# Kernel optimization log

Measured on AMD Instinct MI355X. Metric: run time of the kernel, lower is better.

## Reference

```python
import jax, jax.numpy as jnp
import numpy as np
from jax.scipy.linalg import solve_triangular

S = 64            # number of weight samples (Xi.shape[0])
OUT = 256         # out_channels
IN_CH, K = 64, 3
F = IN_CH * K * K # in_features == inducing_batch == 576
LOG_PREC_INIT = -4.0
LOG_PREC_LR = 1.0


def setup_inputs() -> dict:
    key = jax.random.key(0)
    k1, k2, k3, k4 = jax.random.split(key, 4)
    Xi = jax.random.normal(k1, (S, 128, F), jnp.float32)          # only shape[0] is used
    Xi_param = jax.random.normal(k2, (1, F, F), jnp.float32)      # self.Xi: [1, inducing_batch, in_features]
    u = jax.random.normal(k3, (OUT, F, 1), jnp.float32)           # self.u
    log_prec_scaled = (LOG_PREC_INIT / LOG_PREC_LR) * jnp.ones((1, 1, F), jnp.float32)
    Z = jax.random.normal(k4, (S, OUT, F, 1), jnp.float32)        # internal randn noise, made explicit
    return dict(Xi=Xi, Xi_param=Xi_param, u=u, log_prec_scaled=log_prec_scaled, Z=Z)


def reference(Xi, Xi_param, u, log_prec_scaled, Z):
    S_ = Xi.shape[0]
    Fd = Xi_param.shape[-1]
    O = u.shape[0]
    # log_prec = log_prec_lr * log_prec_scaled  (precs == 1)
    log_prec = LOG_PREC_LR * log_prec_scaled[0]                    # [1, F]
    Xe = jnp.broadcast_to(Xi_param, (S_, Fd, Fd))                  # [S, I, F]
    XiLT = jnp.exp(log_prec) * jnp.swapaxes(Xe, -1, -2)            # [S, F, I]  (prec_L is None branch)
    XiLXi = XiLT @ Xe                                              # [S, F, F]
    XiLY = jnp.einsum('sfi,oi->sfo', XiLT, u[..., 0])              # [S, F, O]  (torch: [S, O, F, 1])
    # NealPrior over in_shape: precision = fan_in * I, fan_in = in_features
    prior_prec = float(Fd)
    prec = XiLXi + prior_prec * jnp.eye(Fd, dtype=XiLXi.dtype)     # [S, F, F]
    L = jnp.linalg.cholesky(prec)
    logdet_prec = 2.0 * jnp.sum(jnp.log(jnp.diagonal(L, axis1=-2, axis2=-1)), -1)  # [S]
    logdet_prec_tot = O * logdet_prec                              # expand(S, O).sum(-1)
    # cholesky_solve(XiLY, L): prec^{-1} XiLY, batched over O via RHS columns
    mean = solve_triangular(L, solve_triangular(L, XiLY, lower=True), lower=True, trans=1)  # [S, F, O]
    Zm = jnp.swapaxes(Z[..., 0], -1, -2)                           # [S, F, O]
    dW = solve_triangular(L, Zm, lower=True, trans=1)              # L^T dW = Z
    sample_fo = mean + dW                                          # [S, F, O]
    sample = jnp.swapaxes(sample_fo, -1, -2)                       # [S, O, F] == self._sample
    # logP = mvnormal_log_prob_unnorm(prior_prec, sample^T):  -0.5 tr(x^T P x) + 0.5*O*logdet(P)
    logP = (-0.5 * prior_prec * jnp.sum(sample_fo ** 2, (-1, -2))
            + 0.5 * O * Fd * jnp.log(jnp.asarray(prior_prec, sample.dtype)))
    logQ = -0.5 * jnp.sum(Z ** 2, (-1, -2, -3)) + 0.5 * logdet_prec_tot
    logpq = logP - logQ                                            # [S]
    return sample, logpq
```

## Files before the change

kernel.cpp:

```cpp
#include <hip/hip_runtime.h>

#define F 576
#define OUTC 256
#define SNUM 64
#define PP 576.0f
#define NBLK 36

typedef unsigned short u16;
typedef __attribute__((ext_vector_type(8))) short short8;
typedef __attribute__((ext_vector_type(4))) float f32x4;

__device__ __forceinline__ u16 f2b_rne(float x) {
  unsigned u = __float_as_uint(x);
  unsigned r = (u + 0x7FFF + ((u >> 16) & 1)) >> 16;
  return (u16)r;
}

__device__ __forceinline__ void gbar(int* cnt, int* gen, int b, int barid) {
  __syncthreads();
  if (threadIdx.x == 0) {
    __builtin_amdgcn_fence(__ATOMIC_RELEASE, "agent");
    __hip_atomic_fetch_add(cnt, 1, __ATOMIC_RELAXED, __HIP_MEMORY_SCOPE_AGENT);
    if (b == 0) {
      int target = barid * NBLK;
      while (__hip_atomic_load(cnt, __ATOMIC_RELAXED, __HIP_MEMORY_SCOPE_AGENT) < target) {
        __builtin_amdgcn_s_sleep(1);
      }
      __builtin_amdgcn_fence(__ATOMIC_ACQUIRE, "agent");
      __builtin_amdgcn_fence(__ATOMIC_RELEASE, "agent");
      __hip_atomic_store(gen, barid, __ATOMIC_RELAXED, __HIP_MEMORY_SCOPE_AGENT);
    } else {
      while (__hip_atomic_load(gen, __ATOMIC_RELAXED, __HIP_MEMORY_SCOPE_AGENT) < barid) {
        __builtin_amdgcn_s_sleep(1);
      }
    }
    __builtin_amdgcn_fence(__ATOMIC_ACQUIRE, "agent");
  }
  __syncthreads();
}

__device__ __forceinline__ void mm16(const float (*As)[68], const float (*Bs)[68],
                                     float acc[4][4], int tx, int ty) {
#pragma unroll
  for (int k = 0; k < 32; ++k) {
    float4 a4 = *(const float4*)&As[k][ty * 4];
    float4 b4 = *(const float4*)&Bs[k][tx * 4];
    float av[4] = {a4.x, a4.y, a4.z, a4.w};
    float bv[4] = {b4.x, b4.y, b4.z, b4.w};
#pragma unroll
    for (int r = 0; r < 4; ++r)
#pragma unroll
      for (int c = 0; c < 4; ++c) acc[r][c] += av[r] * bv[c];
  }
}

__device__ void tile_gemm(const float* __restrict__ A, int lda,
                          const float* __restrict__ B, int ldb,
                          float* __restrict__ C, int ldc,
                          int m0, int n0, int K, float sgn,
                          float (*As)[68], float (*Bs)[68]) {
  int t = threadIdx.x, tx = t & 15, ty = t >> 4;
  float acc[4][4] = {};
  for (int k0 = 0; k0 < K; k0 += 32) {
    int rr = t >> 2, kq = t & 3;
    const float* ap = &A[(m0 + rr) * lda + k0 + kq * 8];
    float4 a0 = *(const float4*)ap;
    float4 a1 = *(const float4*)(ap + 4);
    As[kq*8+0][rr] = a0.x; As[kq*8+1][rr] = a0.y;
    As[kq*8+2][rr] = a0.z; As[kq*8+3][rr] = a0.w;
    As[kq*8+4][rr] = a1.x; As[kq*8+5][rr] = a1.y;
    As[kq*8+6][rr] = a1.z; As[kq*8+7][rr] = a1.w;
    int col = t & 63, kr = t >> 6;
#pragma unroll
    for (int kk = 0; kk < 32; kk += 4)
      Bs[kr + kk][col] = B[(k0 + kr + kk) * ldb + n0 + col];
    __syncthreads();
    mm16(As, Bs, acc, tx, ty);
    __syncthreads();
  }
#pragma unroll
  for (int r = 0; r < 4; ++r)
#pragma unroll
    for (int c = 0; c < 4; ++c)
      C[(m0 + ty*4 + r) * ldc + n0 + tx*4 + c] = sgn * acc[r][c];
}

__device__ void diag_factor(float* Ts ) {
  int t = threadIdx.x;
  __syncthreads();
  if (t < 64) {
    int l = t;
    float r[64];
#pragma unroll
    for (int g = 0; g < 64; ++g) r[g] = Ts[l*66 + g];
#pragma unroll
    for (int j = 0; j < 64; ++j) {
      float d = __shfl(r[j], j, 64);
      float inv = 1.0f / sqrtf(d);
      float c = r[j] * inv;
      r[j] = c;
#pragma unroll
      for (int g = j + 1; g < 64; ++g)
        r[g] = fmaf(-__shfl(c, g, 64), c, r[g]);
    }
#pragma unroll
    for (int g = 0; g < 64; ++g) Ts[l*66 + g] = r[g];
  }
  __syncthreads();
}

__device__ void panel_phase(float* __restrict__ G, int k0, int b,
                            float* Ts, float* invd) {
  int t = threadIdx.x;
  for (int idx = t; idx < 64 * 64; idx += 256) {
    int i = idx >> 6, j = idx & 63;
    Ts[i*66 + j] = G[(k0 + i) * F + k0 + j];
  }
  __syncthreads();
  if (t < 64) invd[t] = 1.0f / Ts[t*66 + t];
  __syncthreads();
  int l = t & 63, w = t >> 6;
  int r0 = k0 + 64 + b * 16 + w * 4;
  float v0 = G[(r0 + 0) * F + k0 + l];
  float v1 = G[(r0 + 1) * F + k0 + l];
  float v2 = G[(r0 + 2) * F + k0 + l];
  float v3 = G[(r0 + 3) * F + k0 + l];
#pragma unroll
  for (int j = 0; j < 64; ++j) {
    float dj = invd[j];
    float x0 = __shfl(v0, j, 64) * dj;
    float x1 = __shfl(v1, j, 64) * dj;
    float x2 = __shfl(v2, j, 64) * dj;
    float x3 = __shfl(v3, j, 64) * dj;
    if (l > j) {
      float lj = Ts[l*66 + j];
      v0 = fmaf(-x0, lj, v0);
      v1 = fmaf(-x1, lj, v1);
      v2 = fmaf(-x2, lj, v2);
      v3 = fmaf(-x3, lj, v3);
    }
  }
  float dl = invd[l];
  G[(r0 + 0) * F + k0 + l] = v0 * dl;
  G[(r0 + 1) * F + k0 + l] = v1 * dl;
  G[(r0 + 2) * F + k0 + l] = v2 * dl;
  G[(r0 + 3) * F + k0 + l] = v3 * dl;
}

__device__ void upd_phase(float* __restrict__ G, int k0, int ti, int tj, bool fuse,
                          float (*As)[68], float (*Bs)[68], float* Ts) {
  int b0 = k0 + 64;
  int i0 = b0 + ti * 64, j0 = b0 + tj * 64;
  int t = threadIdx.x, tx = t & 15, ty = t >> 4;
  float acc[4][4] = {};
  for (int kk0 = 0; kk0 < 64; kk0 += 32) {
    for (int idx = t; idx < 64 * 32; idx += 256) {
      int ii = idx >> 5, kk = idx & 31;
      As[kk][ii] = G[(i0 + ii) * F + k0 + kk0 + kk];
      Bs[kk][ii] = G[(j0 + ii) * F + k0 + kk0 + kk];
    }
    __syncthreads();
#pragma unroll
    for (int k = 0; k < 32; ++k) {
      float a[4], b[4];
#pragma unroll
      for (int m = 0; m < 4; ++m) { a[m] = As[k][ty*4 + m]; b[m] = Bs[k][tx*4 + m]; }
#pragma unroll
      for (int r = 0; r < 4; ++r)
#pragma unroll
        for (int c = 0; c < 4; ++c) acc[r][c] += a[r] * b[c];
    }
    __syncthreads();
  }
  if (!fuse) {
#pragma unroll
    for (int r = 0; r < 4; ++r)
#pragma unroll
      for (int c = 0; c < 4; ++c)
        G[(i0 + ty*4 + r) * F + j0 + tx*4 + c] -= acc[r][c];
  } else {
#pragma unroll
    for (int r = 0; r < 4; ++r)
#pragma unroll
      for (int c = 0; c < 4; ++c)
        Ts[(ty*4 + r)*66 + tx*4 + c] =
            G[(i0 + ty*4 + r) * F + j0 + tx*4 + c] - acc[r][c];
    diag_factor(Ts);
    for (int idx = t; idx < 64 * 64; idx += 256) {
      int i = idx >> 6, j = idx & 63;
      if (j <= i) G[(i0 + i) * F + j0 + j] = Ts[i*66 + j];
    }
  }
}

__device__ void base_inv_phase(const float* __restrict__ G, float* __restrict__ LI,
                               int blk, float* Ts, float* invd) {
  int base = blk * 64, t = threadIdx.x;
  for (int idx = t; idx < 64 * 64; idx += 256) {
    int i = idx >> 6, j = idx & 63;
    Ts[i*66 + j] = G[(base + i) * F + base + j];
  }
  __syncthreads();
  if (t < 64) invd[t] = 1.0f / Ts[t*66 + t];
  __syncthreads();
  int l = t & 63, w = t >> 6;
  float v[16];
#pragma unroll
  for (int c = 0; c < 16; ++c) v[c] = (l == (w * 16 + c)) ? 1.0f : 0.0f;
#pragma unroll
  for (int j = 0; j < 64; ++j) {
    float dj = invd[j];
    float lj = (l > j) ? Ts[l*66 + j] : 0.0f;
#pragma unroll
    for (int c = 0; c < 16; ++c) {
      float x = __shfl(v[c], j, 64) * dj;
      v[c] = fmaf(-x, lj, v[c]);
    }
  }
  float dl = invd[l];
#pragma unroll
  for (int c = 0; c < 16; ++c)
    LI[(base + l) * F + base + w * 16 + c] = v[c] * dl;
}

__device__ void mean_phase(const float* __restrict__ LI, const float* __restrict__ T,
                           float* __restrict__ meanT, int bf, int bo,
                           float (*As)[68], float (*Bs)[68]) {
  int t = threadIdx.x, tx = t & 15, ty = t >> 4;
  int f0 = bf * 64, o0 = bo * 64;
  float acc[4][4] = {};
  for (int g0 = f0; g0 < F; g0 += 32) {
    int col = t & 63, kr = t >> 6;
#pragma unroll
    for (int kk = 0; kk < 32; kk += 4) {
      As[kr + kk][col] = T[(g0 + kr + kk) * OUTC + o0 + col];
      Bs[kr + kk][col] = LI[(g0 + kr + kk) * F + f0 + col];
    }
    __syncthreads();
    mm16(As, Bs, acc, tx, ty);
    __syncthreads();
  }
#pragma unroll
  for (int r = 0; r < 4; ++r) {
    float4 st = make_float4(acc[r][0], acc[r][1], acc[r][2], acc[r][3]);
    *(float4*)&meanT[(o0 + ty*4 + r) * F + f0 + tx*4] = st;
  }
}

__global__ __launch_bounds__(256) void k_mid(float* __restrict__ G, float* __restrict__ LI,
                                             const float* __restrict__ Yb,
                                             float* __restrict__ Tb, float* __restrict__ meanT,
                                             int* __restrict__ cnt, int* __restrict__ gen) {
  __shared__ float As[32][68];
  __shared__ float Bs[32][68];
  __shared__ float Ts[64 * 66];
  __shared__ float invd[64];
  int bar = 0;
  int b = blockIdx.x, t = threadIdx.x;
  float* Tw = Tb;

  if (b == 0) {
    for (int idx = t; idx < 64 * 64; idx += 256) {
      int i = idx >> 6, j = idx & 63;
      Ts[i*66 + j] = G[i * F + j];
    }
    diag_factor(Ts);
    for (int idx = t; idx < 64 * 64; idx += 256) {
      int i = idx >> 6, j = idx & 63;
      if (j <= i) G[i * F + j] = Ts[i*66 + j];
    }
  }
  gbar(cnt, gen, b, ++bar);

  for (int k = 0; k < 8; ++k) {
    int k0 = k * 64;
    int n = 512 - k0;
    if (b < n / 16) panel_phase(G, k0, b, Ts, invd);
    gbar(cnt, gen, b, ++bar);
    int nt = n / 64, ntiles = nt * (nt + 1) / 2;
    if (b < ntiles) {
      int ti = 0, bb = b;
      while (bb >= ti + 1) { bb -= ti + 1; ++ti; }
      int tj = bb;
      upd_phase(G, k0, ti, tj, (ti == 0 && tj == 0), As, Bs, Ts);
    }
    gbar(cnt, gen, b, ++bar);
  }

  if (b < 9) {
    base_inv_phase(G, LI, b, Ts, invd);
  } else {
    int m = b - 9;
    for (int q = m; q < 72; q += 27) {
      int r = q / 8, cc = q % 8;
      int c = cc + (cc >= r ? 1 : 0);
      for (int idx = t; idx < 64 * 16; idx += 256) {
        int i = idx >> 4, jj = idx & 15;
        ((float4*)&LI[(r * 64 + i) * F + c * 64])[jj] = make_float4(0.f, 0.f, 0.f, 0.f);
      }
    }
  }
  gbar(cnt, gen, b, ++bar);

  if (b < 4) {
    tile_gemm(G + 64*F + b*128*(F+1), F, LI + b*128*(F+1), F,
              Tw + b*4096, 64, 0, 0, 64, 1.0f, As, Bs);
    tile_gemm(LI + 64*(F+1) + b*128*(F+1), F, Tw + b*4096, 64,
              LI + 64*F + b*128*(F+1), F, 0, 0, 64, -1.0f, As, Bs);
  }
  gbar(cnt, gen, b, ++bar);
  if (b < 8) {
    int z = b >> 2, tl = b & 3;
    tile_gemm(G + 128*F + z*256*(F+1), F, LI + z*256*(F+1), F,
              Tw + z*16384, 128, (tl>>1)*64, (tl&1)*64, 128, 1.0f, As, Bs);
  }
  gbar(cnt, gen, b, ++bar);
  if (b < 8) {
    int z = b >> 2, tl = b & 3;
    tile_gemm(LI + 128*(F+1) + z*256*(F+1), F, Tw + z*16384, 128,
              LI + 128*F + z*256*(F+1), F, (tl>>1)*64, (tl&1)*64, 128, -1.0f, As, Bs);
  }
  gbar(cnt, gen, b, ++bar);
  if (b < 16) tile_gemm(G + 256*F, F, LI, F, Tw, 256,
                        (b>>2)*64, (b&3)*64, 256, 1.0f, As, Bs);
  gbar(cnt, gen, b, ++bar);
  if (b < 16) tile_gemm(LI + 256*(F+1), F, Tw, 256, LI + 256*F, F,
                        (b>>2)*64, (b&3)*64, 256, -1.0f, As, Bs);
  gbar(cnt, gen, b, ++bar);
  if (b < 8) {
    tile_gemm(G + 512*F, F, LI, F, Tw, 512, 0, b*64, 512, 1.0f, As, Bs);
    tile_gemm(LI + 512*(F+1), F, Tw, 512, LI + 512*F, F, 0, b*64, 64, -1.0f, As, Bs);
  }
  gbar(cnt, gen, b, ++bar);

  {
    int bg = b >> 2, bo = b & 3;
    tile_gemm(LI, F, Yb, OUTC, Tb, OUTC, bg * 64, bo * 64, bg * 64 + 64, 1.0f, As, Bs);
  }
  gbar(cnt, gen, b, ++bar);

  {
    int bf = b >> 2, bo = b & 3;
    mean_phase(LI, Tb, meanT, bf, bo, As, Bs);
  }
}

__global__ __launch_bounds__(256) void k_gy(const float* __restrict__ X,
                                            const float* __restrict__ u,
                                            const float* __restrict__ lp,
                                            float* __restrict__ G,
                                            float* __restrict__ Y) {
  __shared__ float As[32][68];
  __shared__ float Bs[32][68];
  int t = threadIdx.x, tx = t & 15, ty = t >> 4;
  if (blockIdx.z == 0) {
    int bi = blockIdx.y, bj = blockIdx.x;
    if (bj > bi) return;
    int f0 = bi * 64, g0 = bj * 64;
    float acc[4][4] = {};
    for (int i0 = 0; i0 < F; i0 += 32) {
      int col = t & 63, kr = t >> 6;
#pragma unroll
      for (int kk = 0; kk < 32; kk += 4) {
        int i = i0 + kr + kk;
        float e = expf(lp[i]);
        As[kr + kk][col] = e * X[i * F + f0 + col];
        Bs[kr + kk][col] = X[i * F + g0 + col];
      }
      __syncthreads();
      mm16(As, Bs, acc, tx, ty);
      __syncthreads();
    }
#pragma unroll
    for (int r = 0; r < 4; ++r) {
      int gr = f0 + ty*4 + r;
#pragma unroll
      for (int c = 0; c < 4; ++c) {
        int gc = g0 + tx*4 + c;
        float v = acc[r][c];
        if (gr == gc) v += PP;
        G[gr * F + gc] = v;
      }
    }
  } else {
    if (blockIdx.x >= 4) return;
    int bo = blockIdx.x, bf = blockIdx.y;
    int f0 = bf * 64, o0 = bo * 64;
    float acc[4][4] = {};
    for (int i0 = 0; i0 < F; i0 += 32) {
      {
        int col = t & 63, kr = t >> 6;
#pragma unroll
        for (int kk = 0; kk < 32; kk += 4) {
          int i = i0 + kr + kk;
          As[kr + kk][col] = expf(lp[i]) * X[i * F + f0 + col];
        }
        int oo = t >> 2, kq = t & 3;
        const float* ur = &u[(o0 + oo) * F + i0 + kq * 8];
        float4 u0 = *(const float4*)ur;
        float4 u1 = *(const float4*)(ur + 4);
        Bs[kq*8+0][oo] = u0.x; Bs[kq*8+1][oo] = u0.y;
        Bs[kq*8+2][oo] = u0.z; Bs[kq*8+3][oo] = u0.w;
        Bs[kq*8+4][oo] = u1.x; Bs[kq*8+5][oo] = u1.y;
        Bs[kq*8+6][oo] = u1.z; Bs[kq*8+7][oo] = u1.w;
      }
      __syncthreads();
      mm16(As, Bs, acc, tx, ty);
      __syncthreads();
    }
#pragma unroll
    for (int r = 0; r < 4; ++r) {
      float4 st = make_float4(acc[r][0], acc[r][1], acc[r][2], acc[r][3]);
      *(float4*)&Y[(f0 + ty*4 + r) * OUTC + o0 + tx*4] = st;
    }
  }
}

__global__ __launch_bounds__(256) void k_split(const float* __restrict__ LI,
                                               u16* __restrict__ H, u16* __restrict__ L) {
  __shared__ float Tt[64][65];
  int gb = blockIdx.x, fb = blockIdx.y;
  int t = threadIdx.x;
  for (int idx = t; idx < 4096; idx += 256) {
    int i = idx >> 6, j = idx & 63;
    Tt[i][j] = LI[(gb * 64 + i) * F + fb * 64 + j];
  }
  __syncthreads();
  for (int idx = t; idx < 4096; idx += 256) {
    int i = idx >> 6, j = idx & 63;
    float x = Tt[j][i];
    u16 h = f2b_rne(x);
    float hf = __uint_as_float((unsigned)h << 16);
    H[(fb * 64 + i) * F + gb * 64 + j] = h;
    L[(fb * 64 + i) * F + gb * 64 + j] = f2b_rne(x - hf);
  }
}

#define PADK 72
__global__ __launch_bounds__(256) void k_big(const float* __restrict__ Z,
                                             const u16* __restrict__ BHg,
                                             const u16* __restrict__ BLg,
                                             const float* __restrict__ meanT,
                                             float* __restrict__ out,
                                             double* __restrict__ parts) {
  int bf = blockIdx.x, br = blockIdx.y;
  __shared__ u16 ZH[64 * PADK];
  __shared__ u16 ZL[64 * PADK];
  __shared__ u16 BH[64 * PADK];
  __shared__ u16 BL[64 * PADK];
  __shared__ double redA[256];
  __shared__ double redB[256];
  int t = threadIdx.x, l = t & 63, w = t >> 6;
  int f0 = bf * 64, r0 = br * 64;
  int rr = t >> 2, kq = t & 3;
  f32x4 acc0 = {0.f,0.f,0.f,0.f}, acc1 = {0.f,0.f,0.f,0.f};
  f32x4 acc2 = {0.f,0.f,0.f,0.f}, acc3 = {0.f,0.f,0.f,0.f};
  double zsq = 0.0;

  for (int g0 = f0; g0 < F; g0 += 64) {
    {
      const float* zp = &Z[(r0 + rr) * F + g0 + kq * 16];
      float xs[16];
      *(float4*)&xs[0]  = *(const float4*)(zp + 0);
      *(float4*)&xs[4]  = *(const float4*)(zp + 4);
      *(float4*)&xs[8]  = *(const float4*)(zp + 8);
      *(float4*)&xs[12] = *(const float4*)(zp + 12);
      u16 hh[16], ll[16];
#pragma unroll
      for (int j = 0; j < 16; ++j) {
        u16 h = f2b_rne(xs[j]);
        float hf = __uint_as_float((unsigned)h << 16);
        hh[j] = h;
        ll[j] = f2b_rne(xs[j] - hf);
        if (bf == 0) zsq += (double)xs[j] * xs[j];
      }
      *(short8*)&ZH[rr * PADK + kq * 16 + 0] = *(short8*)&hh[0];
      *(short8*)&ZH[rr * PADK + kq * 16 + 8] = *(short8*)&hh[8];
      *(short8*)&ZL[rr * PADK + kq * 16 + 0] = *(short8*)&ll[0];
      *(short8*)&ZL[rr * PADK + kq * 16 + 8] = *(short8*)&ll[8];
      const u16* bh = &BHg[(f0 + rr) * F + g0 + kq * 16];
      const u16* bl = &BLg[(f0 + rr) * F + g0 + kq * 16];
      *(short8*)&BH[rr * PADK + kq * 16 + 0] = *(const short8*)(bh + 0);
      *(short8*)&BH[rr * PADK + kq * 16 + 8] = *(const short8*)(bh + 8);
      *(short8*)&BL[rr * PADK + kq * 16 + 0] = *(const short8*)(bl + 0);
      *(short8*)&BL[rr * PADK + kq * 16 + 8] = *(const short8*)(bl + 8);
    }
    __syncthreads();
#pragma unroll
    for (int kk = 0; kk < 2; ++kk) {
      int aoff = (w * 16 + (l & 15)) * PADK + kk * 32 + (l >> 4) * 8;
      short8 ah = *(short8*)&ZH[aoff];
      short8 al = *(short8*)&ZL[aoff];
      int b0o = ((l & 15)) * PADK + kk * 32 + (l >> 4) * 8;
      {
        short8 bh = *(short8*)&BH[b0o];
        short8 bl = *(short8*)&BL[b0o];
        acc0 = __builtin_amdgcn_mfma_f32_16x16x32_bf16(ah, bh, acc0, 0, 0, 0);
        acc0 = __builtin_amdgcn_mfma_f32_16x16x32_bf16(ah, bl, acc0, 0, 0, 0);
        acc0 = __builtin_amdgcn_mfma_f32_16x16x32_bf16(al, bh, acc0, 0, 0, 0);
      }
      {
        short8 bh = *(short8*)&BH[b0o + 16 * PADK];
        short8 bl = *(short8*)&BL[b0o + 16 * PADK];
        acc1 = __builtin_amdgcn_mfma_f32_16x16x32_bf16(ah, bh, acc1, 0, 0, 0);
        acc1 = __builtin_amdgcn_mfma_f32_16x16x32_bf16(ah, bl, acc1, 0, 0, 0);
        acc1 = __builtin_amdgcn_mfma_f32_16x16x32_bf16(al, bh, acc1, 0, 0, 0);
      }
      {
        short8 bh = *(short8*)&BH[b0o + 32 * PADK];
        short8 bl = *(short8*)&BL[b0o + 32 * PADK];
        acc2 = __builtin_amdgcn_mfma_f32_16x16x32_bf16(ah, bh, acc2, 0, 0, 0);
        acc2 = __builtin_amdgcn_mfma_f32_16x16x32_bf16(ah, bl, acc2, 0, 0, 0);
        acc2 = __builtin_amdgcn_mfma_f32_16x16x32_bf16(al, bh, acc2, 0, 0, 0);
      }
      {
        short8 bh = *(short8*)&BH[b0o + 48 * PADK];
        short8 bl = *(short8*)&BL[b0o + 48 * PADK];
        acc3 = __builtin_amdgcn_mfma_f32_16x16x32_bf16(ah, bh, acc3, 0, 0, 0);
        acc3 = __builtin_amdgcn_mfma_f32_16x16x32_bf16(ah, bl, acc3, 0, 0, 0);
        acc3 = __builtin_amdgcn_mfma_f32_16x16x32_bf16(al, bh, acc3, 0, 0, 0);
      }
    }
    __syncthreads();
  }

  double ssq = 0.0;
  int colb = l & 15, rq = l >> 4;
#pragma unroll
  for (int c = 0; c < 4; ++c) {
    f32x4 a = (c == 0) ? acc0 : (c == 1) ? acc1 : (c == 2) ? acc2 : acc3;
#pragma unroll
    for (int r = 0; r < 4; ++r) {
      int row = r0 + w * 16 + rq * 4 + r;
      int col = f0 + c * 16 + colb;
      float v = a[r] + meanT[(row & 255) * F + col];
      out[row * F + col] = v;
      ssq += (double)v * v;
    }
  }
  redA[t] = ssq; redB[t] = zsq;
  __syncthreads();
  for (int o = 128; o > 0; o >>= 1) {
    if (t < o) { redA[t] += redA[t + o]; redB[t] += redB[t + o]; }
    __syncthreads();
  }
  if (t == 0) {
    int s = br >> 2;
    atomicAdd(&parts[s * 2 + 0], redA[0]);
    if (bf == 0) atomicAdd(&parts[s * 2 + 1], redB[0]);
  }
}

__global__ __launch_bounds__(576) void k_logpq_final(const float* __restrict__ LI,
                                                     const double* __restrict__ parts,
                                                     float* __restrict__ out) {
  __shared__ double red[576];
  int t = threadIdx.x;
  red[t] = log((double)LI[t * F + t]);
  __syncthreads();
  for (int o = 512; o > 0; o >>= 1) {
    if (t < o && t + o < 576) red[t] += red[t + o];
    __syncthreads();
  }
  double ldsumLI = red[0];
  if (t < SNUM) {
    double ssq = parts[t * 2 + 0];
    double zsq = parts[t * 2 + 1];
    double pp = 576.0;
    double lpq = -0.5 * pp * ssq
               + 0.5 * (double)(OUTC * F) * log(pp)
               + 0.5 * zsq
               + (double)OUTC * ldsumLI;
    out[SNUM * OUTC * F + t] = (float)lpq;
  }
}

extern "C" void kernel_launch(void* const* d_in, const int* in_sizes, int n_in,
                              void* d_out, int out_size, void* d_ws, size_t ws_size,
                              hipStream_t stream) {
  (void)in_sizes; (void)n_in; (void)out_size; (void)ws_size;
  const float* X  = (const float*)d_in[1];
  const float* u  = (const float*)d_in[2];
  const float* lp = (const float*)d_in[3];
  const float* Z  = (const float*)d_in[4];
  float* out = (float*)d_out;

  float* ws    = (float*)d_ws;
  float* G     = ws;
  float* LI    = ws + 331776;
  float* Yb    = ws + 663552;
  float* Tb    = ws + 811008;
  float* meanT = ws + 958464;
  double* parts = (double*)(ws + 1105920);
  int*    cnt   = (int*)(ws + 1105920 + 256);
  int*    gen   = (int*)(ws + 1105920 + 288);
  u16* LIT_H = (u16*)G;
  u16* LIT_L = LIT_H + 331776;

  hipMemsetAsync((void*)(ws + 1105920), 0, 1416, stream);
  k_gy<<<dim3(9, 9, 2), 256, 0, stream>>>(X, u, lp, G, Yb);
  k_mid<<<NBLK, 256, 0, stream>>>(G, LI, Yb, Tb, meanT, cnt, gen);
  k_split<<<dim3(9, 9), 256, 0, stream>>>(LI, LIT_H, LIT_L);
  k_big<<<dim3(9, 256), 256, 0, stream>>>(Z, LIT_H, LIT_L, meanT, out, parts);
  k_logpq_final<<<1, 576, 0, stream>>>(LI, parts, out);
}
```

Measured before the change: 648.8 us.

## Switch blocked Cholesky to 128-wide panels to halve grid barriers

Restructures the in-kernel blocked Cholesky from 64-wide to 128-wide panels. The diagonal 128x128 block is factored entirely in LDS by one workgroup (two 64 factors plus an internal trailing update), and the trailing update is split into regular tiles and a fused diagonal tile. This cuts the number of grid-wide barrier phases from 17 to 9. In exchange, the single-block diagonal factorization becomes longer and more serial, and LDS use grows to about 66KB, which may reduce occupancy.

```diff
diff --git a/kernel.cpp b/kernel.cpp
--- a/kernel.cpp
+++ b/kernel.cpp
@@ -5,6 +5,7 @@
 #define SNUM 64
 #define PP 576.0f
 #define NBLK 36
+#define TS 130
 
 typedef unsigned short u16;
 typedef __attribute__((ext_vector_type(8))) short short8;
@@ -85,14 +86,14 @@
       C[(m0 + ty*4 + r) * ldc + n0 + tx*4 + c] = sgn * acc[r][c];
 }
 
-__device__ void diag_factor(float* Ts ) {
+__device__ void diag_factor_g(float* Ts, int base) {
   int t = threadIdx.x;
   __syncthreads();
   if (t < 64) {
     int l = t;
     float r[64];
 #pragma unroll
-    for (int g = 0; g < 64; ++g) r[g] = Ts[l*66 + g];
+    for (int g = 0; g < 64; ++g) r[g] = Ts[(base + l) * TS + base + g];
 #pragma unroll
     for (int j = 0; j < 64; ++j) {
       float d = __shfl(r[j], j, 64);
@@ -104,56 +105,142 @@
         r[g] = fmaf(-__shfl(c, g, 64), c, r[g]);
     }
 #pragma unroll
-    for (int g = 0; g < 64; ++g) Ts[l*66 + g] = r[g];
-  }
-  __syncthreads();
-}
-
-__device__ void panel_phase(float* __restrict__ G, int k0, int b,
-                            float* Ts, float* invd) {
+    for (int g = 0; g < 64; ++g) Ts[(base + l) * TS + base + g] = r[g];
+  }
+  __syncthreads();
+}
+
+__device__ void factor128_lds(float* Ts, float* invd) {
+  int t = threadIdx.x, l = t & 63, w = t >> 6;
+  diag_factor_g(Ts, 0);
+  if (t < 64) invd[t] = 1.0f / Ts[t * TS + t];
+  __syncthreads();
+  for (int pass = 0; pass < 4; ++pass) {
+    int r = 64 + w * 16 + pass * 4;
+    float v0 = Ts[(r + 0) * TS + l];
+    float v1 = Ts[(r + 1) * TS + l];
+    float v2 = Ts[(r + 2) * TS + l];
+    float v3 = Ts[(r + 3) * TS + l];
+#pragma unroll
+    for (int j = 0; j < 64; ++j) {
+      float dj = invd[j];
+      float x0 = __shfl(v0, j, 64) * dj;
+      float x1 = __shfl(v1, j, 64) * dj;
+      float x2 = __shfl(v2, j, 64) * dj;
+      float x3 = __shfl(v3, j, 64) * dj;
+      if (l > j) {
+        float lj = Ts[l * TS + j];
+        v0 = fmaf(-x0, lj, v0);
+        v1 = fmaf(-x1, lj, v1);
+        v2 = fmaf(-x2, lj, v2);
+        v3 = fmaf(-x3, lj, v3);
+      }
+    }
+    float dl = invd[l];
+    Ts[(r + 0) * TS + l] = v0 * dl;
+    Ts[(r + 1) * TS + l] = v1 * dl;
+    Ts[(r + 2) * TS + l] = v2 * dl;
+    Ts[(r + 3) * TS + l] = v3 * dl;
+  }
+  __syncthreads();
+  int tx = t & 15, ty = t >> 4;
+  float acc[4][4] = {};
+#pragma unroll 8
+  for (int k = 0; k < 64; ++k) {
+    float a[4], bb[4];
+#pragma unroll
+    for (int m = 0; m < 4; ++m) {
+      a[m]  = Ts[(64 + ty * 4 + m) * TS + k];
+      bb[m] = Ts[(64 + tx * 4 + m) * TS + k];
+    }
+#pragma unroll
+    for (int r = 0; r < 4; ++r)
+#pragma unroll
+      for (int c = 0; c < 4; ++c) acc[r][c] += a[r] * bb[c];
+  }
+  __syncthreads();
+#pragma unroll
+  for (int r = 0; r < 4; ++r)
+#pragma unroll
+    for (int c = 0; c < 4; ++c)
+      Ts[(64 + ty * 4 + r) * TS + 64 + tx * 4 + c] -= acc[r][c];
+  diag_factor_g(Ts, 64);
+}
+
+__device__ void panel128_phase(float* __restrict__ G, int k0, int b,
+                               float* Ts, float* invd) {
   int t = threadIdx.x;
-  for (int idx = t; idx < 64 * 64; idx += 256) {
-    int i = idx >> 6, j = idx & 63;
-    Ts[i*66 + j] = G[(k0 + i) * F + k0 + j];
-  }
-  __syncthreads();
-  if (t < 64) invd[t] = 1.0f / Ts[t*66 + t];
+  for (int idx = t; idx < 128 * 128; idx += 256) {
+    int i = idx >> 7, j = idx & 127;
+    Ts[i * TS + j] = G[(k0 + i) * F + k0 + j];
+  }
+  __syncthreads();
+  if (t < 128) invd[t] = 1.0f / Ts[t * TS + t];
   __syncthreads();
   int l = t & 63, w = t >> 6;
-  int r0 = k0 + 64 + b * 16 + w * 4;
-  float v0 = G[(r0 + 0) * F + k0 + l];
-  float v1 = G[(r0 + 1) * F + k0 + l];
-  float v2 = G[(r0 + 2) * F + k0 + l];
-  float v3 = G[(r0 + 3) * F + k0 + l];
+  int r0 = k0 + 128 + b * 16 + w * 4;
+  float va0 = G[(r0 + 0) * F + k0 + l];
+  float va1 = G[(r0 + 1) * F + k0 + l];
+  float va2 = G[(r0 + 2) * F + k0 + l];
+  float va3 = G[(r0 + 3) * F + k0 + l];
+  float vb0 = G[(r0 + 0) * F + k0 + 64 + l];
+  float vb1 = G[(r0 + 1) * F + k0 + 64 + l];
+  float vb2 = G[(r0 + 2) * F + k0 + 64 + l];
+  float vb3 = G[(r0 + 3) * F + k0 + 64 + l];
 #pragma unroll
   for (int j = 0; j < 64; ++j) {
     float dj = invd[j];
-    float x0 = __shfl(v0, j, 64) * dj;
-    float x1 = __shfl(v1, j, 64) * dj;
-    float x2 = __shfl(v2, j, 64) * dj;
-    float x3 = __shfl(v3, j, 64) * dj;
+    float x0 = __shfl(va0, j, 64) * dj;
+    float x1 = __shfl(va1, j, 64) * dj;
+    float x2 = __shfl(va2, j, 64) * dj;
+    float x3 = __shfl(va3, j, 64) * dj;
     if (l > j) {
-      float lj = Ts[l*66 + j];
-      v0 = fmaf(-x0, lj, v0);
-      v1 = fmaf(-x1, lj, v1);
-      v2 = fmaf(-x2, lj, v2);
-      v3 = fmaf(-x3, lj, v3);
-    }
-  }
-  float dl = invd[l];
-  G[(r0 + 0) * F + k0 + l] = v0 * dl;
-  G[(r0 + 1) * F + k0 + l] = v1 * dl;
-  G[(r0 + 2) * F + k0 + l] = v2 * dl;
-  G[(r0 + 3) * F + k0 + l] = v3 * dl;
-}
-
-__device__ void upd_phase(float* __restrict__ G, int k0, int ti, int tj, bool fuse,
-                          float (*As)[68], float (*Bs)[68], float* Ts) {
-  int b0 = k0 + 64;
+      float lj = Ts[l * TS + j];
+      va0 = fmaf(-x0, lj, va0);
+      va1 = fmaf(-x1, lj, va1);
+      va2 = fmaf(-x2, lj, va2);
+      va3 = fmaf(-x3, lj, va3);
+    }
+    float lj2 = Ts[(64 + l) * TS + j];
+    vb0 = fmaf(-x0, lj2, vb0);
+    vb1 = fmaf(-x1, lj2, vb1);
+    vb2 = fmaf(-x2, lj2, vb2);
+    vb3 = fmaf(-x3, lj2, vb3);
+  }
+#pragma unroll
+  for (int j = 64; j < 128; ++j) {
+    int jj = j - 64;
+    float dj = invd[j];
+    float x0 = __shfl(vb0, jj, 64) * dj;
+    float x1 = __shfl(vb1, jj, 64) * dj;
+    float x2 = __shfl(vb2, jj, 64) * dj;
+    float x3 = __shfl(vb3, jj, 64) * dj;
+    if (l > jj) {
+      float lj = Ts[(64 + l) * TS + j];
+      vb0 = fmaf(-x0, lj, vb0);
+      vb1 = fmaf(-x1, lj, vb1);
+      vb2 = fmaf(-x2, lj, vb2);
+      vb3 = fmaf(-x3, lj, vb3);
+    }
+  }
+  float dla = invd[l], dlb = invd[64 + l];
+  G[(r0 + 0) * F + k0 + l] = va0 * dla;
+  G[(r0 + 1) * F + k0 + l] = va1 * dla;
+  G[(r0 + 2) * F + k0 + l] = va2 * dla;
+  G[(r0 + 3) * F + k0 + l] = va3 * dla;
+  G[(r0 + 0) * F + k0 + 64 + l] = vb0 * dlb;
+  G[(r0 + 1) * F + k0 + 64 + l] = vb1 * dlb;
+  G[(r0 + 2) * F + k0 + 64 + l] = vb2 * dlb;
+  G[(r0 + 3) * F + k0 + 64 + l] = vb3 * dlb;
+}
+
+__device__ void upd128_phase(float* __restrict__ G, int k0, int ti, int tj,
+                             float (*As)[68], float (*Bs)[68]) {
+  int b0 = k0 + 128;
   int i0 = b0 + ti * 64, j0 = b0 + tj * 64;
   int t = threadIdx.x, tx = t & 15, ty = t >> 4;
   float acc[4][4] = {};
-  for (int kk0 = 0; kk0 < 64; kk0 += 32) {
+  for (int kk0 = 0; kk0 < 128; kk0 += 32) {
     for (int idx = t; idx < 64 * 32; idx += 256) {
       int ii = idx >> 5, kk = idx & 31;
       As[kk][ii] = G[(i0 + ii) * F + k0 + kk0 + kk];
@@ -162,34 +249,106 @@
     __syncthreads();
 #pragma unroll
     for (int k = 0; k < 32; ++k) {
-      float a[4], b[4];
-#pragma unroll
-      for (int m = 0; m < 4; ++m) { a[m] = As[k][ty*4 + m]; b[m] = Bs[k][tx*4 + m]; }
+      float a[4], bb[4];
+#pragma unroll
+      for (int m = 0; m < 4; ++m) { a[m] = As[k][ty*4 + m]; bb[m] = Bs[k][tx*4 + m]; }
 #pragma unroll
       for (int r = 0; r < 4; ++r)
 #pragma unroll
-        for (int c = 0; c < 4; ++c) acc[r][c] += a[r] * b[c];
-    }
-    __syncthreads();
-  }
-  if (!fuse) {
-#pragma unroll
-    for (int r = 0; r < 4; ++r)
-#pragma unroll
-      for (int c = 0; c < 4; ++c)
-        G[(i0 + ty*4 + r) * F + j0 + tx*4 + c] -= acc[r][c];
+        for (int c = 0; c < 4; ++c) acc[r][c] += a[r] * bb[c];
+    }
+    __syncthreads();
+  }
+#pragma unroll
+  for (int r = 0; r < 4; ++r)
+#pragma unroll
+    for (int c = 0; c < 4; ++c)
+      G[(i0 + ty*4 + r) * F + j0 + tx*4 + c] -= acc[r][c];
+}
+
+__device__ void fused_diag128(float* __restrict__ G, int k0, int d0,
+                              float* Ts, float* invd, float (*As)[68], float (*Bs)[68]) {
+  int t = threadIdx.x, tx = t & 15, ty = t >> 4;
+  if (k0 < 0) {
+    for (int idx = t; idx < 128 * 128; idx += 256) {
+      int i = idx >> 7, j = idx & 127;
+      Ts[i * TS + j] = G[(d0 + i) * F + d0 + j];
+    }
   } else {
-#pragma unroll
-    for (int r = 0; r < 4; ++r)
-#pragma unroll
-      for (int c = 0; c < 4; ++c)
-        Ts[(ty*4 + r)*66 + tx*4 + c] =
-            G[(i0 + ty*4 + r) * F + j0 + tx*4 + c] - acc[r][c];
-    diag_factor(Ts);
-    for (int idx = t; idx < 64 * 64; idx += 256) {
-      int i = idx >> 6, j = idx & 63;
-      if (j <= i) G[(i0 + i) * F + j0 + j] = Ts[i*66 + j];
-    }
+    const int pa[3] = {0, 1, 1}, pb[3] = {0, 0, 1};
+#pragma unroll
+    for (int s = 0; s < 3; ++s) {
+      int a = pa[s], bq = pb[s];
+      int i0 = d0 + a * 64, j0 = d0 + bq * 64;
+      float acc[4][4] = {};
+      for (int kk0 = 0; kk0 < 128; kk0 += 32) {
+        __syncthreads();
+        for (int idx = t; idx < 64 * 32; idx += 256) {
+          int ii = idx >> 5, kk = idx & 31;
+          As[kk][ii] = G[(i0 + ii) * F + k0 + kk0 + kk];
+          Bs[kk][ii] = G[(j0 + ii) * F + k0 + kk0 + kk];
+        }
+        __syncthreads();
+#pragma unroll
+        for (int k = 0; k < 32; ++k) {
+          float av[4], bv[4];
+#pragma unroll
+          for (int m = 0; m < 4; ++m) { av[m] = As[k][ty*4 + m]; bv[m] = Bs[k][tx*4 + m]; }
+#pragma unroll
+          for (int r = 0; r < 4; ++r)
+#pragma unroll
+            for (int c = 0; c < 4; ++c) acc[r][c] += av[r] * bv[c];
+        }
+      }
+      __syncthreads();
+#pragma unroll
+      for (int r = 0; r < 4; ++r)
+#pragma unroll
+        for (int c = 0; c < 4; ++c)
+          Ts[(a * 64 + ty*4 + r) * TS + bq * 64 + tx*4 + c] =
+              G[(i0 + ty*4 + r) * F + j0 + tx*4 + c] - acc[r][c];
+    }
+  }
+  factor128_lds(Ts, invd);
+  for (int idx = t; idx < 128 * 128; idx += 256) {
+    int i = idx >> 7, j = idx & 127;
+    if (j <= i) G[(d0 + i) * F + d0 + j] = Ts[i * TS + j];
+  }
+}
+
+__device__ void fused_diag64(float* __restrict__ G, int k0, int d0,
+                             float* Ts, float (*As)[68], float (*Bs)[68]) {
+  int t = threadIdx.x, tx = t & 15, ty = t >> 4;
+  float acc[4][4] = {};
+  for (int kk0 = 0; kk0 < 128; kk0 += 32) {
+    __syncthreads();
+    for (int idx = t; idx < 64 * 32; idx += 256) {
+      int ii = idx >> 5, kk = idx & 31;
+      As[kk][ii] = G[(d0 + ii) * F + k0 + kk0 + kk];
+    }
+    __syncthreads();
+#pragma unroll
+    for (int k = 0; k < 32; ++k) {
+      float av[4], bv[4];
+#pragma unroll
+      for (int m = 0; m < 4; ++m) { av[m] = As[k][ty*4 + m]; bv[m] = As[k][tx*4 + m]; }
+#pragma unroll
+      for (int r = 0; r < 4; ++r)
+#pragma unroll
+        for (int c = 0; c < 4; ++c) acc[r][c] += av[r] * bv[c];
+    }
+  }
+  __syncthreads();
+#pragma unroll
+  for (int r = 0; r < 4; ++r)
+#pragma unroll
+    for (int c = 0; c < 4; ++c)
+      Ts[(ty*4 + r) * TS + tx*4 + c] =
+          G[(d0 + ty*4 + r) * F + d0 + tx*4 + c] - acc[r][c];
+  diag_factor_g(Ts, 0);
+  for (int idx = t; idx < 64 * 64; idx += 256) {
+    int i = idx >> 6, j = idx & 63;
+    if (j <= i) G[(d0 + i) * F + d0 + j] = Ts[i * TS + j];
   }
 }
 
@@ -198,10 +357,10 @@
   int base = blk * 64, t = threadIdx.x;
   for (int idx = t; idx < 64 * 64; idx += 256) {
     int i = idx >> 6, j = idx & 63;
-    Ts[i*66 + j] = G[(base + i) * F + base + j];
-  }
-  __syncthreads();
-  if (t < 64) invd[t] = 1.0f / Ts[t*66 + t];
+    Ts[i * TS + j] = G[(base + i) * F + base + j];
+  }
+  __syncthreads();
+  if (t < 64) invd[t] = 1.0f / Ts[t * TS + t];
   __syncthreads();
   int l = t & 63, w = t >> 6;
   float v[16];
@@ -210,7 +369,7 @@
 #pragma unroll
   for (int j = 0; j < 64; ++j) {
     float dj = invd[j];
-    float lj = (l > j) ? Ts[l*66 + j] : 0.0f;
+    float lj = (l > j) ? Ts[l * TS + j] : 0.0f;
 #pragma unroll
     for (int c = 0; c < 16; ++c) {
       float x = __shfl(v[c], j, 64) * dj;
@@ -253,36 +412,31 @@
                                              int* __restrict__ cnt, int* __restrict__ gen) {
   __shared__ float As[32][68];
   __shared__ float Bs[32][68];
-  __shared__ float Ts[64 * 66];
-  __shared__ float invd[64];
+  __shared__ float Ts[128 * TS];
+  __shared__ float invd[128];
   int bar = 0;
   int b = blockIdx.x, t = threadIdx.x;
   float* Tw = Tb;
 
-  if (b == 0) {
-    for (int idx = t; idx < 64 * 64; idx += 256) {
-      int i = idx >> 6, j = idx & 63;
-      Ts[i*66 + j] = G[i * F + j];
-    }
-    diag_factor(Ts);
-    for (int idx = t; idx < 64 * 64; idx += 256) {
-      int i = idx >> 6, j = idx & 63;
-      if (j <= i) G[i * F + j] = Ts[i*66 + j];
-    }
-  }
-  gbar(cnt, gen, b, ++bar);
-
-  for (int k = 0; k < 8; ++k) {
-    int k0 = k * 64;
-    int n = 512 - k0;
-    if (b < n / 16) panel_phase(G, k0, b, Ts, invd);
+  if (b == 35) fused_diag128(G, -1, 0, Ts, invd, As, Bs);
+  gbar(cnt, gen, b, ++bar);
+
+  for (int k = 0; k < 4; ++k) {
+    int k0 = k * 128;
+    int nb_p = (576 - k0 - 128) / 16;
+    if (b < nb_p) panel128_phase(G, k0, b, Ts, invd);
     gbar(cnt, gen, b, ++bar);
-    int nt = n / 64, ntiles = nt * (nt + 1) / 2;
-    if (b < ntiles) {
-      int ti = 0, bb = b;
-      while (bb >= ti + 1) { bb -= ti + 1; ++ti; }
-      int tj = bb;
-      upd_phase(G, k0, ti, tj, (ti == 0 && tj == 0), As, Bs, Ts);
+    if (k < 3) {
+      int nt = (576 - k0 - 128) / 64;
+      int nreg = nt * (nt + 1) / 2 - 3;
+      if (b < nreg) {
+        int ti = 2, bb = b;
+        while (bb >= ti + 1) { bb -= ti + 1; ++ti; }
+        upd128_phase(G, k0, ti, bb, As, Bs);
+      }
+      if (b == 35) fused_diag128(G, k0, k0 + 128, Ts, invd, As, Bs);
+    } else {
+      if (b == 35) fused_diag64(G, k0, 512, Ts, As, Bs);
     }
     gbar(cnt, gen, b, ++bar);
   }
```

Result: slower. 840.3 us (+29.5%).
